# Kernel tuning notes

Measured on AMD Instinct MI355X. Metric: run time of the kernel, lower is better.

The kernel has to match this reference:

```python
import jax, jax.numpy as jnp
import numpy as np

IN_F = 4096
OUT_F = 4096
GROUP = 128                      # quantization group size
NG = IN_F * OUT_F // GROUP       # 131072 groups
LORA_R = 16
LORA_SCALE = 32.0 / 16.0         # lora_alpha / lora_r


def _dequant(indices, codebook, scales):
    # Unpack two INT4 nibbles per byte: low nibble first, then high (interleaved).
    low = indices & 15
    high = (indices >> 4) & 15
    idx = jnp.stack([low, high], axis=1).reshape(-1)          # [numel]
    # Codebook lookup, per-group scaling.
    vals = codebook[idx].reshape(NG, GROUP) * scales[:, None]  # [NG, GROUP]
    return vals.reshape(OUT_F, IN_F)


def setup_inputs() -> dict:
    key = jax.random.key(0)
    ks = jax.random.split(key, 7)
    return {
        "x": jax.random.normal(ks[0], (4, 2048, IN_F), dtype=jnp.float32),
        "indices": jax.random.randint(ks[1], (IN_F * OUT_F // 2,), 0, 256, dtype=jnp.int32),
        "codebook": jax.random.normal(ks[2], (16,), dtype=jnp.float32),
        "scales": jax.random.uniform(ks[3], (NG,), dtype=jnp.float32, minval=0.01, maxval=1.0),
        "lora_A": jax.random.normal(ks[4], (IN_F, LORA_R), dtype=jnp.float32) / 64.0,
        "lora_B": jax.random.normal(ks[5], (LORA_R, OUT_F), dtype=jnp.float32) / 64.0,
        "bias": jax.random.normal(ks[6], (OUT_F,), dtype=jnp.float32),
    }


def reference(x, indices, codebook, scales, lora_A, lora_B, bias):
    # lowram path: dequantize INT4 codebook weights, F.linear, fused LoRA add, bias.
    W = _dequant(indices, codebook, scales)                    # [OUT_F, IN_F]
    h = jnp.einsum('bsi,oi->bso', x, W)                        # F.linear (no bias yet)
    h = h + (x @ lora_A) @ lora_B * LORA_SCALE                 # LoRA adapter (dropout=0)
    return h + bias
```

## Files before the change

kernel.cpp:

```cpp
#include <hip/hip_runtime.h>
#include <stdint.h>

#define IN_F   4096
#define OUT_F  4096
#define M_TOT  8192
#define KDIM   4096

typedef float          f32x4  __attribute__((ext_vector_type(4)));
typedef int            i32x4  __attribute__((ext_vector_type(4)));
typedef unsigned short u16x8  __attribute__((ext_vector_type(8)));
typedef __bf16         bf16x8 __attribute__((ext_vector_type(8)));

__device__ __forceinline__ unsigned short f2bf(float f) {
  uint32_t u = __builtin_bit_cast(uint32_t, f);
  u = (u + 0x7FFFu + ((u >> 16) & 1u)) >> 16;
  return (unsigned short)u;
}
__device__ __forceinline__ float bf2f(unsigned short s) {
  return __builtin_bit_cast(float, (uint32_t)s << 16);
}

__device__ __forceinline__ void gld_lds16(const void* g, void* l) {
  __builtin_amdgcn_global_load_lds((const __attribute__((address_space(1))) void*)g,
                                   (__attribute__((address_space(3))) void*)l,
                                   16, 0, 0);
}

__global__ __launch_bounds__(256) void k_xcast(const f32x4* __restrict__ x,
                                               u16x8* __restrict__ xb) {
  int t = blockIdx.x * 256 + threadIdx.x;
  f32x4 a = x[2 * t];
  f32x4 b = x[2 * t + 1];
  u16x8 o;
  o[0] = f2bf(a[0]); o[1] = f2bf(a[1]); o[2] = f2bf(a[2]); o[3] = f2bf(a[3]);
  o[4] = f2bf(b[0]); o[5] = f2bf(b[1]); o[6] = f2bf(b[2]); o[7] = f2bf(b[3]);
  xb[t] = o;
}

__global__ __launch_bounds__(256) void k_lora(const float* __restrict__ A,
                                              const float* __restrict__ Bm,
                                              unsigned short* __restrict__ L) {
  __shared__ float sB[16][64];
  const int ib = blockIdx.x * 256;
  const int ob = blockIdx.y * 64;
  const int t  = threadIdx.x;
  for (int j = 0; j < 4; ++j) {
    int idx = t + j * 256;
    int r = idx >> 6, oc = idx & 63;
    sB[r][oc] = Bm[r * OUT_F + ob + oc];
  }
  float a[16];
  const f32x4* Ap = (const f32x4*)(A + (size_t)(ib + t) * 16);
  #pragma unroll
  for (int j = 0; j < 4; ++j) {
    f32x4 v = Ap[j];
    a[4*j+0] = v[0]; a[4*j+1] = v[1]; a[4*j+2] = v[2]; a[4*j+3] = v[3];
  }
  __syncthreads();
  unsigned short* Lp = L + (size_t)ob * IN_F + ib + t;
  #pragma unroll 4
  for (int oc = 0; oc < 64; ++oc) {
    float acc = 0.f;
    #pragma unroll
    for (int r = 0; r < 16; ++r) acc += a[r] * sB[r][oc];
    Lp[(size_t)oc * IN_F] = f2bf(acc * 2.0f);
  }
}

__global__ __launch_bounds__(256) void k_dequant(const int* __restrict__ idx,
                                                 const float* __restrict__ cb,
                                                 const float* __restrict__ scales,
                                                 const unsigned short* __restrict__ L,
                                                 unsigned short* __restrict__ Wc) {
  __shared__ float scb[16];
  const int t = blockIdx.x * 256 + threadIdx.x;
  if (threadIdx.x < 16) scb[threadIdx.x] = cb[threadIdx.x];
  __syncthreads();
  i32x4 w = ((const i32x4*)idx)[t];
  float sc = scales[t >> 4];
  u16x8 lw = ((const u16x8*)L)[t];
  u16x8 o;
  #pragma unroll
  for (int j = 0; j < 4; ++j) {
    int word = w[j];
    float v0 = scb[word & 15] * sc + bf2f(lw[2 * j]);
    float v1 = scb[(word >> 4) & 15] * sc + bf2f(lw[2 * j + 1]);
    o[2 * j]     = f2bf(v0);
    o[2 * j + 1] = f2bf(v1);
  }
  ((u16x8*)Wc)[t] = o;
}


#define BARR()  __builtin_amdgcn_s_barrier()
#define LGKM0() asm volatile("s_waitcnt lgkmcnt(0)" ::: "memory")
#define VMC0()  asm volatile("s_waitcnt vmcnt(0)" ::: "memory")

#define STAGE_A(kt, ha, c) do {                                                          \
  gld_lds16(Ag + (size_t)((ha) * 128) * KDIM + (kt) * 64,                                \
            smem + (c) * 32768 + (ha) * 16384 + ldsw);                                   \
  gld_lds16(Ag + (size_t)((ha) * 128 + 64) * KDIM + (kt) * 64,                           \
            smem + (c) * 32768 + (ha) * 16384 + 8192 + ldsw);                            \
} while (0)

#define STAGE_B(kt, hb, c) do {                                                          \
  gld_lds16(Bg + (size_t)((hb) * 128) * KDIM + (kt) * 64,                                \
            smem + 65536 + (c) * 32768 + (hb) * 16384 + ldsw);                           \
  gld_lds16(Bg + (size_t)((hb) * 128 + 64) * KDIM + (kt) * 64,                           \
            smem + 65536 + (c) * 32768 + (hb) * 16384 + 8192 + ldsw);                    \
} while (0)

#define LOAD_AH(DST, qm, c) do {                                                         \
  const char* _p = smem + (c) * 32768 + rowA + (qm) * 8192;                              \
  _Pragma("unroll")                                                                      \
  for (int mi = 0; mi < 4; ++mi) {                                                       \
    DST[mi][0] = *(const bf16x8*)(_p + mi * 2048 + coff0);                               \
    DST[mi][1] = *(const bf16x8*)(_p + mi * 2048 + coff1);                               \
  }                                                                                      \
} while (0)

#define LOAD_B(c) do {                                                                   \
  const char* _p = smem + 65536 + (c) * 32768 + rowB;                                    \
  _Pragma("unroll")                                                                      \
  for (int ni = 0; ni < 4; ++ni) {                                                       \
    bfr[ni][0] = *(const bf16x8*)(_p + ni * 2048 + coff0);                               \
    bfr[ni][1] = *(const bf16x8*)(_p + ni * 2048 + coff1);                               \
  }                                                                                      \
} while (0)

#define MFMA_PH(qm, nb, AF) do {                                                         \
  __builtin_amdgcn_s_setprio(1);                                                         \
  _Pragma("unroll")                                                                      \
  for (int mi = 0; mi < 4; ++mi)                                                         \
    _Pragma("unroll")                                                                    \
    for (int nj = 0; nj < 2; ++nj)                                                       \
      _Pragma("unroll")                                                                  \
      for (int kk = 0; kk < 2; ++kk)                                                     \
        acc[(qm) * 4 + mi][(nb) * 2 + nj] = __builtin_amdgcn_mfma_f32_16x16x32_bf16(     \
            AF[mi][kk], bfr[(nb) * 2 + nj][kk], acc[(qm) * 4 + mi][(nb) * 2 + nj],       \
            0, 0, 0);                                                                    \
  __builtin_amdgcn_s_setprio(0);                                                         \
} while (0)

#define TILE2(t_, c_, doStage) do {                                                      \
  if (doStage) {                                                                         \
    STAGE_B((t_) + 1, 0, (c_) ^ 1); STAGE_B((t_) + 1, 1, (c_) ^ 1);                      \
    STAGE_A((t_) + 1, 0, (c_) ^ 1); STAGE_A((t_) + 1, 1, (c_) ^ 1);                      \
  }                                                                                      \
  LOAD_AH(afA, 0, c_); LOAD_B(c_); LOAD_AH(afB, 1, c_);                                  \
  MFMA_PH(0, 0, afA); MFMA_PH(0, 1, afA);                                                \
  MFMA_PH(1, 1, afB); MFMA_PH(1, 0, afB);                                                \
  LGKM0(); VMC0(); BARR();                                                               \
} while (0)

__global__ __launch_bounds__(512, 2) void k_gemm(const unsigned short* __restrict__ A,
                                                 const unsigned short* __restrict__ B,
                                                 const float* __restrict__ bias,
                                                 float* __restrict__ C) {
  __shared__ char smem[131072];
  const int tid  = threadIdx.x;
  const int lane = tid & 63;
  const int wv   = tid >> 6;
  const int wm   = wv >> 2;
  const int wn   = wv & 3;
  const int r    = lane & 15;
  const int q    = lane >> 4;
  const int xr   = r & 7;
  const int coff0 = (q ^ xr) << 4;
  const int coff1 = ((q + 4) ^ xr) << 4;
  const int rowA = (wm * 128 + r) * 128;
  const int rowB = (wn * 64 + r) * 128;
  const int srow = tid >> 3;
  const int scol = ((tid & 7) ^ ((tid >> 3) & 7)) * 8;
  const int ldsw = wv * 1024;
  const int bm = blockIdx.x;
  const int bn = blockIdx.y;

  const unsigned short* Ag = A + (size_t)(bm * 256 + srow) * KDIM + scol;
  const unsigned short* Bg = B + (size_t)(bn * 256 + srow) * KDIM + scol;

  bf16x8 afA[4][2], afB[4][2], bfr[4][2];
  f32x4 acc[8][4];
  #pragma unroll
  for (int m = 0; m < 8; ++m)
    #pragma unroll
    for (int n = 0; n < 4; ++n)
      acc[m][n] = (f32x4){0.f, 0.f, 0.f, 0.f};

  STAGE_B(0, 0, 0); STAGE_B(0, 1, 0); STAGE_A(0, 0, 0); STAGE_A(0, 1, 0);
  VMC0();
  BARR();

  #pragma unroll 1
  for (int t = 0; t < 62; t += 2) {
    TILE2(t,     0, 1);
    TILE2(t + 1, 1, 1);
  }
  TILE2(62, 0, 1);
  TILE2(63, 1, 0);

  __syncthreads();
  {
    char* eps = smem + wv * 4096;
    const int row0 = bm * 256 + wm * 128;
    const int col0 = bn * 256 + wn * 64;
    const f32x4 bias4 = *(const f32x4*)(bias + col0 + r * 4);
    #pragma unroll
    for (int mi = 0; mi < 8; ++mi) {
      #pragma unroll
      for (int j = 0; j < 4; ++j)
        #pragma unroll
        for (int ni = 0; ni < 4; ++ni)
          *(float*)(eps + (((q * 4 + j) * 64) + ni * 16 + r) * 4) = acc[mi][ni][j];
      LGKM0();
      __builtin_amdgcn_sched_barrier(0);
      #pragma unroll
      for (int p = 0; p < 4; ++p) {
        const int row = p * 4 + q;
        f32x4 v = *(const f32x4*)(eps + row * 256 + r * 16);
        v[0] += bias4[0]; v[1] += bias4[1]; v[2] += bias4[2]; v[3] += bias4[3];
        *(f32x4*)(C + (size_t)(row0 + mi * 16 + row) * OUT_F + col0 + r * 4) = v;
      }
      asm volatile("" ::: "memory");
    }
  }
}

extern "C" void kernel_launch(void* const* d_in, const int* in_sizes, int n_in,
                              void* d_out, int out_size, void* d_ws, size_t ws_size,
                              hipStream_t stream) {
  const float* x    = (const float*)d_in[0];
  const int*   idx  = (const int*)d_in[1];
  const float* cb   = (const float*)d_in[2];
  const float* scl  = (const float*)d_in[3];
  const float* lA   = (const float*)d_in[4];
  const float* lB   = (const float*)d_in[5];
  const float* bias = (const float*)d_in[6];
  float* out = (float*)d_out;

  unsigned short* xb = (unsigned short*)d_ws;
  unsigned short* Wc = (unsigned short*)((char*)d_ws + (size_t)M_TOT * KDIM * 2);
  unsigned short* Lbuf = (unsigned short*)d_out;

  k_xcast<<<16384, 256, 0, stream>>>((const f32x4*)x, (u16x8*)xb);
  k_lora<<<dim3(16, 64), 256, 0, stream>>>(lA, lB, Lbuf);
  k_dequant<<<8192, 256, 0, stream>>>(idx, cb, scl, Lbuf, Wc);
  k_gemm<<<dim3(32, 16), 512, 0, stream>>>(xb, Wc, bias, out);
}
```

Before: 280.5 us.

## Load B fragments directly from global into registers, halve LDS

```diff
diff --git a/kernel.cpp b/kernel.cpp
--- a/kernel.cpp
+++ b/kernel.cpp
@@ -103,53 +103,40 @@
             smem + (c) * 32768 + (ha) * 16384 + 8192 + ldsw);                            \
 } while (0)
 
-#define STAGE_B(kt, hb, c) do {                                                          \
-  gld_lds16(Bg + (size_t)((hb) * 128) * KDIM + (kt) * 64,                                \
-            smem + 65536 + (c) * 32768 + (hb) * 16384 + ldsw);                           \
-  gld_lds16(Bg + (size_t)((hb) * 128 + 64) * KDIM + (kt) * 64,                           \
-            smem + 65536 + (c) * 32768 + (hb) * 16384 + 8192 + ldsw);                    \
-} while (0)
-
-#define LOAD_AH(DST, qm, c) do {                                                         \
-  const char* _p = smem + (c) * 32768 + rowA + (qm) * 8192;                              \
+#define BLOAD(DST, kt, kkk) do {                                                         \
   _Pragma("unroll")                                                                      \
-  for (int mi = 0; mi < 4; ++mi) {                                                       \
-    DST[mi][0] = *(const bf16x8*)(_p + mi * 2048 + coff0);                               \
-    DST[mi][1] = *(const bf16x8*)(_p + mi * 2048 + coff1);                               \
-  }                                                                                      \
-} while (0)
-
-#define LOAD_B(c) do {                                                                   \
-  const char* _p = smem + 65536 + (c) * 32768 + rowB;                                    \
+  for (int n = 0; n < 4; ++n)                                                            \
+    DST[n] = *(const bf16x8*)(Bv + (size_t)n * 16 * KDIM + (size_t)(kt) * 64 + (kkk) * 32); \
+} while (0)
+
+#define READ_AF(DST, c, COFF) do {                                                       \
+  const char* _p = smem + (c) * 32768 + rowA;                                            \
   _Pragma("unroll")                                                                      \
-  for (int ni = 0; ni < 4; ++ni) {                                                       \
-    bfr[ni][0] = *(const bf16x8*)(_p + ni * 2048 + coff0);                               \
-    bfr[ni][1] = *(const bf16x8*)(_p + ni * 2048 + coff1);                               \
-  }                                                                                      \
-} while (0)
-
-#define MFMA_PH(qm, nb, AF) do {                                                         \
+  for (int m16 = 0; m16 < 8; ++m16)                                                      \
+    DST[m16] = *(const bf16x8*)(_p + m16 * 2048 + (COFF));                               \
+} while (0)
+
+#define MFMA_32(AF, BF) do {                                                             \
   __builtin_amdgcn_s_setprio(1);                                                         \
   _Pragma("unroll")                                                                      \
-  for (int mi = 0; mi < 4; ++mi)                                                         \
+  for (int m16 = 0; m16 < 8; ++m16)                                                      \
     _Pragma("unroll")                                                                    \
-    for (int nj = 0; nj < 2; ++nj)                                                       \
-      _Pragma("unroll")                                                                  \
-      for (int kk = 0; kk < 2; ++kk)                                                     \
-        acc[(qm) * 4 + mi][(nb) * 2 + nj] = __builtin_amdgcn_mfma_f32_16x16x32_bf16(     \
-            AF[mi][kk], bfr[(nb) * 2 + nj][kk], acc[(qm) * 4 + mi][(nb) * 2 + nj],       \
-            0, 0, 0);                                                                    \
+    for (int n = 0; n < 4; ++n)                                                          \
+      acc[m16][n] = __builtin_amdgcn_mfma_f32_16x16x32_bf16(AF[m16], BF[n],              \
+                                                            acc[m16][n], 0, 0, 0);      \
   __builtin_amdgcn_s_setprio(0);                                                         \
 } while (0)
 
-#define TILE2(t_, c_, doStage) do {                                                      \
+#define TILE3(t_, c_, BC0, BN0, doStage) do {                                            \
+  BLOAD(bK1, (t_), 1);                                                                   \
   if (doStage) {                                                                         \
-    STAGE_B((t_) + 1, 0, (c_) ^ 1); STAGE_B((t_) + 1, 1, (c_) ^ 1);                      \
+    BLOAD(BN0, (t_) + 1, 0);                                                             \
     STAGE_A((t_) + 1, 0, (c_) ^ 1); STAGE_A((t_) + 1, 1, (c_) ^ 1);                      \
   }                                                                                      \
-  LOAD_AH(afA, 0, c_); LOAD_B(c_); LOAD_AH(afB, 1, c_);                                  \
-  MFMA_PH(0, 0, afA); MFMA_PH(0, 1, afA);                                                \
-  MFMA_PH(1, 1, afB); MFMA_PH(1, 0, afB);                                                \
+  READ_AF(af0, c_, coff0);                                                               \
+  MFMA_32(af0, BC0);                                                                     \
+  READ_AF(af1, c_, coff1);                                                               \
+  MFMA_32(af1, bK1);                                                                     \
   LGKM0(); VMC0(); BARR();                                                               \
 } while (0)
 
@@ -157,7 +144,7 @@
                                                  const unsigned short* __restrict__ B,
                                                  const float* __restrict__ bias,
                                                  float* __restrict__ C) {
-  __shared__ char smem[131072];
+  __shared__ char smem[65536];
   const int tid  = threadIdx.x;
   const int lane = tid & 63;
   const int wv   = tid >> 6;
@@ -169,7 +156,6 @@
   const int coff0 = (q ^ xr) << 4;
   const int coff1 = ((q + 4) ^ xr) << 4;
   const int rowA = (wm * 128 + r) * 128;
-  const int rowB = (wn * 64 + r) * 128;
   const int srow = tid >> 3;
   const int scol = ((tid & 7) ^ ((tid >> 3) & 7)) * 8;
   const int ldsw = wv * 1024;
@@ -177,9 +163,9 @@
   const int bn = blockIdx.y;
 
   const unsigned short* Ag = A + (size_t)(bm * 256 + srow) * KDIM + scol;
-  const unsigned short* Bg = B + (size_t)(bn * 256 + srow) * KDIM + scol;
-
-  bf16x8 afA[4][2], afB[4][2], bfr[4][2];
+  const unsigned short* Bv = B + (size_t)(bn * 256 + wn * 64 + r) * KDIM + q * 8;
+
+  bf16x8 af0[8], af1[8], bK0a[4], bK0b[4], bK1[4];
   f32x4 acc[8][4];
   #pragma unroll
   for (int m = 0; m < 8; ++m)
@@ -187,17 +173,18 @@
     for (int n = 0; n < 4; ++n)
       acc[m][n] = (f32x4){0.f, 0.f, 0.f, 0.f};
 
-  STAGE_B(0, 0, 0); STAGE_B(0, 1, 0); STAGE_A(0, 0, 0); STAGE_A(0, 1, 0);
+  BLOAD(bK0a, 0, 0);
+  STAGE_A(0, 0, 0); STAGE_A(0, 1, 0);
   VMC0();
   BARR();
 
   #pragma unroll 1
   for (int t = 0; t < 62; t += 2) {
-    TILE2(t,     0, 1);
-    TILE2(t + 1, 1, 1);
-  }
-  TILE2(62, 0, 1);
-  TILE2(63, 1, 0);
+    TILE3(t,     0, bK0a, bK0b, 1);
+    TILE3(t + 1, 1, bK0b, bK0a, 1);
+  }
+  TILE3(62, 0, bK0a, bK0b, 1);
+  TILE3(63, 1, bK0b, bK0a, 0);
 
   __syncthreads();
   {
```

After: 429.9 us. +53.3%, slower.
